# Kernel optimization log

Hardware: AMD Instinct MI355X
Metric: run time of the kernel (lower is better)

## Reference

```python
import jax, jax.numpy as jnp
import numpy as np

ROPE_THETA = 10000.0

def _rope(x, offset=0):
    # x: [B, H, T, d]; lucidrains rotary_embedding_torch interleaved-pair convention
    d = x.shape[-1]
    T = x.shape[-2]
    inv_freq = 1.0 / (ROPE_THETA ** (jnp.arange(0, d, 2, dtype=jnp.float32) / d))  # [d/2]
    t = jnp.arange(offset, offset + T, dtype=jnp.float32)
    freqs = t[:, None] * inv_freq[None, :]                 # [T, d/2]
    freqs = jnp.repeat(freqs, 2, axis=-1)                  # [T, d] (each freq duplicated for its pair)
    cos = jnp.cos(freqs).astype(x.dtype)
    sin = jnp.sin(freqs).astype(x.dtype)
    xr = x.reshape(*x.shape[:-1], d // 2, 2)
    x1, x2 = xr[..., 0], xr[..., 1]
    rot = jnp.stack([-x2, x1], axis=-1).reshape(x.shape)   # rotate_half, interleaved
    return x * cos + rot * sin


def setup_inputs() -> dict:
    key = jax.random.key(0)
    ks = jax.random.split(key, 5)
    B, T, C = 8, 1024, 1024
    s = 0.02
    x = jax.random.normal(ks[0], (B, T, C), dtype=jnp.float32)
    ipw = jax.random.normal(ks[1], (3 * C, C), dtype=jnp.float32) * s
    ipb = jax.random.normal(ks[2], (3 * C,), dtype=jnp.float32) * s
    opw = jax.random.normal(ks[3], (C, C), dtype=jnp.float32) * s
    opb = jax.random.normal(ks[4], (C,), dtype=jnp.float32) * s
    # bool mask, True = blocked (original code inverts before SDPA) -> causal
    causal_block = ~jnp.tril(jnp.ones((T, T), dtype=bool))
    attn_mask = causal_block[None, None, :, :]             # [1,1,T,T]
    return {"x": x, "ipw": ipw, "ipb": ipb, "opw": opw, "opb": opb,
            "attn_mask": attn_mask}


def reference(x, ipw, ipb, opw, opb, attn_mask):
    B, T, C = x.shape
    n_head = 16
    hd = C // n_head
    qkv = x @ ipw.T + ipb                                  # [B,T,3C]
    q, k, v = jnp.split(qkv, 3, axis=-1)
    def heads(z):
        return z.reshape(B, T, n_head, hd).transpose(0, 2, 1, 3)  # [B,H,T,hd]
    q, k, v = heads(q), heads(k), heads(v)
    q = _rope(q)
    k = _rope(k)
    scores = jnp.einsum('bhqd,bhkd->bhqk', q, k) / jnp.sqrt(jnp.asarray(hd, x.dtype))
    # attn_mask True = blocked; mask slice [FULL_T-T:FULL_T, :FULL_T] is the full mask here
    scores = jnp.where(attn_mask, jnp.asarray(-1e9, x.dtype), scores)
    attn = jax.nn.softmax(scores, axis=-1)
    y = jnp.einsum('bhqk,bhkd->bhqd', attn, v)             # [B,H,T,hd]
    y = y.transpose(0, 2, 1, 3).reshape(B, T, C)
    return y @ opw.T + opb
```

## Files before the change

kernel.cpp:

```cpp
#include <hip/hip_runtime.h>
#include <stdint.h>


typedef __bf16 bf16x8 __attribute__((ext_vector_type(8)));
typedef float f32x4 __attribute__((ext_vector_type(4)));
typedef __attribute__((address_space(1))) unsigned int as1_u32;
typedef __attribute__((address_space(3))) unsigned int as3_u32;

#define MFMA16(a, b, c) __builtin_amdgcn_mfma_f32_16x16x32_bf16((a), (b), (c), 0, 0, 0)

static __device__ __forceinline__ unsigned short f2bf(float f) {
    union { float f; unsigned u; } x; x.f = f;
    return (unsigned short)((x.u + 0x7fffu + ((x.u >> 16) & 1u)) >> 16);
}
static __device__ __forceinline__ float bf2f(unsigned short u) {
    union { unsigned u; float f; } x; x.u = ((unsigned)u) << 16;
    return x.f;
}
static __device__ __forceinline__ bf16x8 ld_bf16x8(const void* p) {
    return *(const bf16x8*)p;
}

__global__ void cast_f32_bf16(const float* __restrict__ in,
                              unsigned short* __restrict__ out, int n8) {
    int i = blockIdx.x * blockDim.x + threadIdx.x;
    if (i >= n8) return;
    float4 a = ((const float4*)in)[2 * i];
    float4 b = ((const float4*)in)[2 * i + 1];
    union { unsigned short us[8]; uint4 v; } o;
    o.us[0] = f2bf(a.x); o.us[1] = f2bf(a.y); o.us[2] = f2bf(a.z); o.us[3] = f2bf(a.w);
    o.us[4] = f2bf(b.x); o.us[5] = f2bf(b.y); o.us[6] = f2bf(b.z); o.us[7] = f2bf(b.w);
    ((uint4*)out)[i] = o.v;
}

__global__ void rope_table(float* __restrict__ ct, float* __restrict__ st) {
    int idx = blockIdx.x * blockDim.x + threadIdx.x;
    if (idx >= 1024 * 32) return;
    int t = idx >> 5, i = idx & 31;
    float inv = powf(10000.0f, -(float)(2 * i) * (1.0f / 64.0f));
    float f = (float)t * inv;
    ct[idx] = cosf(f);
    st[idx] = sinf(f);
}

template <int NC, bool OUT_BF16>
__global__ __launch_bounds__(256) void gemm_bt(const unsigned short* __restrict__ A,
                                               const unsigned short* __restrict__ W,
                                               const float* __restrict__ bias,
                                               void* __restrict__ Cout, int K) {
    __shared__ __attribute__((aligned(16))) unsigned short As[128 * 32];
    __shared__ __attribute__((aligned(16))) unsigned short Bs[128 * 32];

    constexpr int NT = NC / 128;
    int nwg = gridDim.x;
    int bid = blockIdx.x;
    int lg = (bid & 7) * (nwg >> 3) + (bid >> 3);
    int tm = lg / NT, tn = lg % NT;
    int m0 = tm * 128, n0 = tn * 128;

    int tid = threadIdx.x;
    int w = tid >> 6, l = tid & 63;
    int lr = l & 15, g = l >> 4;
    int ldsb = __builtin_amdgcn_readfirstlane(w * 512);

    int c0 = tid, c1 = tid + 256;
    const unsigned short* A0 = A + (size_t)(m0 + (c0 >> 2)) * K + (c0 & 3) * 8;
    const unsigned short* A1 = A + (size_t)(m0 + (c1 >> 2)) * K + (c1 & 3) * 8;
    const unsigned short* W0 = W + (size_t)(n0 + (c0 >> 2)) * K + (c0 & 3) * 8;
    const unsigned short* W1 = W + (size_t)(n0 + (c1 >> 2)) * K + (c1 & 3) * 8;

    f32x4 acc[4][4] = {};
    int wr = (w >> 1) * 64, wc = (w & 1) * 64;

    for (int k0 = 0; k0 < K; k0 += 32) {
        __syncthreads();
        __builtin_amdgcn_global_load_lds((const as1_u32*)(A0 + k0), (as3_u32*)(As + ldsb), 16, 0, 0);
        __builtin_amdgcn_global_load_lds((const as1_u32*)(A1 + k0), (as3_u32*)(As + 2048 + ldsb), 16, 0, 0);
        __builtin_amdgcn_global_load_lds((const as1_u32*)(W0 + k0), (as3_u32*)(Bs + ldsb), 16, 0, 0);
        __builtin_amdgcn_global_load_lds((const as1_u32*)(W1 + k0), (as3_u32*)(Bs + 2048 + ldsb), 16, 0, 0);
        __syncthreads();

        bf16x8 a[4], b[4];
#pragma unroll
        for (int i = 0; i < 4; ++i) a[i] = ld_bf16x8(As + (wr + i * 16 + lr) * 32 + g * 8);
#pragma unroll
        for (int j = 0; j < 4; ++j) b[j] = ld_bf16x8(Bs + (wc + j * 16 + lr) * 32 + g * 8);
#pragma unroll
        for (int i = 0; i < 4; ++i)
#pragma unroll
            for (int j = 0; j < 4; ++j) acc[i][j] = MFMA16(a[i], b[j], acc[i][j]);
    }

    int g4 = g * 4;
#pragma unroll
    for (int j = 0; j < 4; ++j) {
        int col = n0 + wc + j * 16 + lr;
        float bv = bias[col];
#pragma unroll
        for (int i = 0; i < 4; ++i) {
#pragma unroll
            for (int r = 0; r < 4; ++r) {
                int row = m0 + wr + i * 16 + g4 + r;
                float v = acc[i][j][r] + bv;
                if (OUT_BF16)
                    ((unsigned short*)Cout)[(size_t)row * NC + col] = f2bf(v);
                else
                    ((float*)Cout)[(size_t)row * NC + col] = v;
            }
        }
    }
}

__global__ void rope_reshape(const unsigned short* __restrict__ qkv,
                             const float* __restrict__ ct, const float* __restrict__ st,
                             unsigned short* __restrict__ Qh,
                             unsigned short* __restrict__ Kh,
                             unsigned short* __restrict__ Vh) {
    int idx = blockIdx.x * blockDim.x + threadIdx.x;
    if (idx >= 8192 * 384) return;
    int row = idx / 384;
    int c8 = idx - row * 384;
    int col = c8 * 8;
    int sec = col >> 10;
    int wi = col & 1023;
    int h = wi >> 6, d = wi & 63;
    int t = row & 1023;

    uint4 raw = *(const uint4*)(qkv + (size_t)row * 3072 + col);
    size_t obase = ((size_t)((row >> 10) * 16 + h) * 1024 + t) * 64 + d;

    if (sec == 2) {
        *(uint4*)(Vh + obase) = raw;
        return;
    }
    union { uint4 v; unsigned short us[8]; } u; u.v = raw;
    float x[8];
#pragma unroll
    for (int i = 0; i < 8; ++i) x[i] = bf2f(u.us[i]);
    float scale = (sec == 0) ? 0.125f : 1.0f;
    union { uint4 v; unsigned short us[8]; } o;
#pragma unroll
    for (int p = 0; p < 4; ++p) {
        int fi = t * 32 + (d >> 1) + p;
        float c = ct[fi], s = st[fi];
        float e0 = (x[2 * p] * c - x[2 * p + 1] * s) * scale;
        float e1 = (x[2 * p + 1] * c + x[2 * p] * s) * scale;
        o.us[2 * p] = f2bf(e0);
        o.us[2 * p + 1] = f2bf(e1);
    }
    unsigned short* dst = (sec == 0) ? Qh : Kh;
    *(uint4*)(dst + obase) = o.v;
}

__global__ __launch_bounds__(256) void attn_fwd(const unsigned short* __restrict__ Qh,
                                                const unsigned short* __restrict__ Kh,
                                                const unsigned short* __restrict__ Vh,
                                                unsigned short* __restrict__ Yb) {
    __shared__ __attribute__((aligned(16))) unsigned short Ks[64 * 64];
    __shared__ __attribute__((aligned(16))) unsigned short Vts[64 * 64];
    __shared__ __attribute__((aligned(16))) unsigned short Ps[4 * 16 * 64];

    int bid = blockIdx.x;
    int lg = (bid & 7) * 256 + (bid >> 3);
    int bh = lg >> 4;
    int qi = lg & 15;
    int q0 = qi * 64;

    int tid = threadIdx.x, w = tid >> 6, l = tid & 63;
    int lr = l & 15, g = l >> 4;
    int ldsb = __builtin_amdgcn_readfirstlane(w * 512);

    const unsigned short* Kbase = Kh + (size_t)bh * 65536;
    const unsigned short* Vbase = Vh + (size_t)bh * 65536;

    bf16x8 qf0, qf1;
    {
        const unsigned short* qp = Qh + (size_t)bh * 65536 + (size_t)(q0 + w * 16 + lr) * 64 + g * 8;
        qf0 = ld_bf16x8(qp);
        qf1 = ld_bf16x8(qp + 32);
    }

    f32x4 y[4] = {};
    float run_m[4], run_l[4];
#pragma unroll
    for (int r = 0; r < 4; ++r) { run_m[r] = -1e30f; run_l[r] = 0.0f; }

    int c0 = tid, c1 = tid + 256;
    const unsigned short* K0 = Kbase + (size_t)(c0 >> 3) * 64 + ((c0 ^ (c0 >> 3)) & 7) * 8;
    const unsigned short* K1 = Kbase + (size_t)(c1 >> 3) * 64 + ((c1 ^ (c1 >> 3)) & 7) * 8;
    int vr = tid >> 2, vd0 = (tid & 3) * 16;
    const unsigned short* V0 = Vbase + (size_t)vr * 64 + vd0;
    unsigned short* Pw = Ps + w * 1024;

    for (int j = 0; j <= qi; ++j) {
        int kvoff = j * 4096;
        __syncthreads();
        __builtin_amdgcn_global_load_lds((const as1_u32*)(K0 + kvoff), (as3_u32*)(Ks + ldsb), 16, 0, 0);
        __builtin_amdgcn_global_load_lds((const as1_u32*)(K1 + kvoff), (as3_u32*)(Ks + 2048 + ldsb), 16, 0, 0);
        uint4 v0 = *(const uint4*)(V0 + kvoff);
        uint4 v1 = *(const uint4*)(V0 + kvoff + 8);
        {
            union { uint4 v[2]; unsigned short us[16]; } u; u.v[0] = v0; u.v[1] = v1;
#pragma unroll
            for (int i = 0; i < 16; ++i) {
                int d = vd0 + i;
                int off = d * 128 + ((((vr >> 3) ^ d) & 7) << 4) + ((vr & 7) << 1);
                *(unsigned short*)((char*)Vts + off) = u.us[i];
            }
        }
        __syncthreads();

        f32x4 s[4];
#pragma unroll
        for (int nt = 0; nt < 4; ++nt) {
            int row = nt * 16 + lr;
            bf16x8 kf0 = ld_bf16x8((const char*)Ks + row * 128 + (((g + 0) ^ (row & 7)) << 4));
            bf16x8 kf1 = ld_bf16x8((const char*)Ks + row * 128 + (((g + 4) ^ (row & 7)) << 4));
            f32x4 z = {};
            z = MFMA16(qf0, kf0, z);
            z = MFMA16(qf1, kf1, z);
            s[nt] = z;
        }

        if (j == qi) {
#pragma unroll
            for (int nt = 0; nt < 4; ++nt) {
                int kv = nt * 16 + lr;
#pragma unroll
                for (int r = 0; r < 4; ++r) {
                    int qrow = w * 16 + g * 4 + r;
                    s[nt][r] = (kv > qrow) ? -1e30f : s[nt][r];
                }
            }
        }

#pragma unroll
        for (int r = 0; r < 4; ++r) {
            float tm_ = fmaxf(fmaxf(s[0][r], s[1][r]), fmaxf(s[2][r], s[3][r]));
            tm_ = fmaxf(tm_, __shfl_xor(tm_, 1));
            tm_ = fmaxf(tm_, __shfl_xor(tm_, 2));
            tm_ = fmaxf(tm_, __shfl_xor(tm_, 4));
            tm_ = fmaxf(tm_, __shfl_xor(tm_, 8));
            float nm = fmaxf(run_m[r], tm_);
            float alpha = __expf(run_m[r] - nm);
            run_m[r] = nm;
            float ts = 0.0f;
#pragma unroll
            for (int nt = 0; nt < 4; ++nt) {
                float pv = __expf(s[nt][r] - nm);
                s[nt][r] = pv;
                ts += pv;
            }
            ts += __shfl_xor(ts, 1);
            ts += __shfl_xor(ts, 2);
            ts += __shfl_xor(ts, 4);
            ts += __shfl_xor(ts, 8);
            run_l[r] = run_l[r] * alpha + ts;
#pragma unroll
            for (int nt = 0; nt < 4; ++nt) y[nt][r] *= alpha;
        }

#pragma unroll
        for (int nt = 0; nt < 4; ++nt)
#pragma unroll
            for (int r = 0; r < 4; ++r) {
                int m = g * 4 + r;
                int col = nt * 16 + lr;
                int off = m * 128 + ((((col >> 3) ^ m) & 7) << 4) + ((col & 7) << 1);
                *(unsigned short*)((char*)Pw + off) = f2bf(s[nt][r]);
            }

#pragma unroll
        for (int ks = 0; ks < 2; ++ks) {
            int slot = (g + ks * 4) ^ (lr & 7);
            bf16x8 pa = ld_bf16x8((const char*)Pw + lr * 128 + slot * 16);
#pragma unroll
            for (int nt = 0; nt < 4; ++nt) {
                int d = nt * 16 + lr;
                int vs = ((g + ks * 4) ^ d) & 7;
                bf16x8 vb = ld_bf16x8((const char*)Vts + d * 128 + (vs << 4));
                y[nt] = MFMA16(pa, vb, y[nt]);
            }
        }
    }

    int b = bh >> 4, h = bh & 15;
#pragma unroll
    for (int r = 0; r < 4; ++r) {
        float inv = 1.0f / run_l[r];
        int row = q0 + w * 16 + g * 4 + r;
        size_t obase = ((size_t)(b * 1024 + row)) * 1024 + h * 64;
#pragma unroll
        for (int nt = 0; nt < 4; ++nt) Yb[obase + nt * 16 + lr] = f2bf(y[nt][r] * inv);
    }
}

extern "C" void kernel_launch(void* const* d_in, const int* in_sizes, int n_in,
                              void* d_out, int out_size, void* d_ws, size_t ws_size,
                              hipStream_t stream) {
    const float* x = (const float*)d_in[0];
    const float* ipw = (const float*)d_in[1];
    const float* ipb = (const float*)d_in[2];
    const float* opw = (const float*)d_in[3];
    const float* opb = (const float*)d_in[4];

    char* ws = (char*)d_ws;
    unsigned short* xb   = (unsigned short*)(ws);
    unsigned short* wqkv = (unsigned short*)(ws + 16777216);
    unsigned short* wo   = (unsigned short*)(ws + 23068672);
    float* ct            = (float*)(ws + 25165824);
    float* st            = (float*)(ws + 25296896);
    unsigned short* qkvb = (unsigned short*)(ws + 25427968);
    unsigned short* Qh   = (unsigned short*)(ws + 75759616);
    unsigned short* Kh   = (unsigned short*)(ws + 92536832);
    unsigned short* Vh   = (unsigned short*)(ws + 109314048);
    unsigned short* yb   = (unsigned short*)(ws + 126091264);

    cast_f32_bf16<<<4096, 256, 0, stream>>>(x, xb, 1048576);
    cast_f32_bf16<<<1536, 256, 0, stream>>>(ipw, wqkv, 393216);
    cast_f32_bf16<<<512, 256, 0, stream>>>(opw, wo, 131072);
    rope_table<<<128, 256, 0, stream>>>(ct, st);

    gemm_bt<3072, true><<<1536, 256, 0, stream>>>(xb, wqkv, ipb, qkvb, 1024);
    rope_reshape<<<12288, 256, 0, stream>>>(qkvb, ct, st, Qh, Kh, Vh);
    attn_fwd<<<2048, 256, 0, stream>>>(Qh, Kh, Vh, yb);
    gemm_bt<1024, false><<<512, 256, 0, stream>>>(yb, wo, opb, d_out, 1024);
}
```

Before: 324.0 us.

## Pair causal query tiles per block, pre-transpose V, keep P in registers

The attention kernel now gives each block two query tiles (p and 15-p), so causal work is balanced across blocks and each loaded K/V tile is reused by both. V is transposed into a separate buffer by a new kernel, which lets it be loaded with direct global-to-LDS copies instead of scalar transposed LDS stores. Scores are computed as K·Q so the softmax probabilities stay in registers as the MFMA operand, removing the LDS round trip for P. Row reductions shrink to two shuffles, and the output is staged through LDS for coalesced stores. The cost is an extra transpose launch, more registers per thread and half as many blocks.

```diff
diff --git a/kernel.cpp b/kernel.cpp
--- a/kernel.cpp
+++ b/kernel.cpp
@@ -19,6 +19,11 @@
 }
 static __device__ __forceinline__ bf16x8 ld_bf16x8(const void* p) {
     return *(const bf16x8*)p;
+}
+static __device__ __forceinline__ unsigned cvtpk(float lo, float hi) {
+    unsigned r;
+    asm("v_cvt_pk_bf16_f32 %0, %1, %2" : "=v"(r) : "v"(lo), "v"(hi));
+    return r;
 }
 
 __global__ void cast_f32_bf16(const float* __restrict__ in,
@@ -114,13 +119,11 @@
 __global__ void rope_reshape(const unsigned short* __restrict__ qkv,
                              const float* __restrict__ ct, const float* __restrict__ st,
                              unsigned short* __restrict__ Qh,
-                             unsigned short* __restrict__ Kh,
-                             unsigned short* __restrict__ Vh) {
+                             unsigned short* __restrict__ Kh) {
     int idx = blockIdx.x * blockDim.x + threadIdx.x;
-    if (idx >= 8192 * 384) return;
-    int row = idx / 384;
-    int c8 = idx - row * 384;
-    int col = c8 * 8;
+    if (idx >= 8192 * 256) return;
+    int row = idx >> 8;
+    int col = (idx & 255) * 8;
     int sec = col >> 10;
     int wi = col & 1023;
     int h = wi >> 6, d = wi & 63;
@@ -129,10 +132,6 @@
     uint4 raw = *(const uint4*)(qkv + (size_t)row * 3072 + col);
     size_t obase = ((size_t)((row >> 10) * 16 + h) * 1024 + t) * 64 + d;
 
-    if (sec == 2) {
-        *(uint4*)(Vh + obase) = raw;
-        return;
-    }
     union { uint4 v; unsigned short us[8]; } u; u.v = raw;
     float x[8];
 #pragma unroll
@@ -152,147 +151,177 @@
     *(uint4*)(dst + obase) = o.v;
 }
 
+__global__ __launch_bounds__(256) void transpose_v(const unsigned short* __restrict__ qkv,
+                                                   unsigned short* __restrict__ Vt) {
+    __shared__ unsigned short Ts[64 * 67];
+    int bid = blockIdx.x;
+    int bh = bid >> 4, tt = bid & 15;
+    int b = bh >> 4, h = bh & 15;
+    int t0 = tt * 64;
+    int tid = threadIdx.x;
+#pragma unroll
+    for (int cc = 0; cc < 2; ++cc) {
+        int c = tid + cc * 256;
+        int trow = c >> 3, d8 = (c & 7) * 8;
+        uint4 v = *(const uint4*)(qkv + (size_t)(b * 1024 + t0 + trow) * 3072 + 2048 + h * 64 + d8);
+        union { uint4 v; unsigned short us[8]; } u; u.v = v;
+#pragma unroll
+        for (int i = 0; i < 8; ++i) Ts[trow * 67 + d8 + i] = u.us[i];
+    }
+    __syncthreads();
+#pragma unroll
+    for (int cc = 0; cc < 2; ++cc) {
+        int c = tid + cc * 256;
+        int drow = c >> 3, t8 = (c & 7) * 8;
+        union { uint4 v; unsigned short us[8]; } u;
+#pragma unroll
+        for (int i = 0; i < 8; ++i) u.us[i] = Ts[(t8 + i) * 67 + drow];
+        *(uint4*)(Vt + (size_t)bh * 65536 + (size_t)drow * 1024 + t0 + t8) = u.v;
+    }
+}
+
+__device__ __forceinline__ void attn_tile(const unsigned short* Ks, const unsigned short* Vs,
+                                          bf16x8 q0f, bf16x8 q1f, f32x4 (&y)[4],
+                                          float& rm, float& rl,
+                                          int lr, int g, bool diag, int wq) {
+    const char* kc = (const char*)Ks;
+    const char* vc = (const char*)Vs;
+    int l7 = lr & 7;
+    int kof0 = lr * 128 + ((g ^ l7) << 4);
+    int kof1 = lr * 128 + (((g + 4) ^ l7) << 4);
+    f32x4 s[4];
+#pragma unroll
+    for (int nt = 0; nt < 4; ++nt) {
+        bf16x8 kf0 = ld_bf16x8(kc + nt * 2048 + kof0);
+        bf16x8 kf1 = ld_bf16x8(kc + nt * 2048 + kof1);
+        f32x4 z = {};
+        z = MFMA16(kf0, q0f, z);
+        z = MFMA16(kf1, q1f, z);
+        s[nt] = z;
+    }
+    if (diag) {
+#pragma unroll
+        for (int nt = 0; nt < 4; ++nt)
+#pragma unroll
+            for (int r = 0; r < 4; ++r)
+                if (nt * 16 + g * 4 + r > wq + lr) s[nt][r] = -3e38f;
+    }
+    float tm;
+    {
+        f32x4 m4;
+#pragma unroll
+        for (int r = 0; r < 4; ++r) m4[r] = fmaxf(fmaxf(s[0][r], s[1][r]), fmaxf(s[2][r], s[3][r]));
+        tm = fmaxf(fmaxf(m4[0], m4[1]), fmaxf(m4[2], m4[3]));
+    }
+    tm = fmaxf(tm, __shfl_xor(tm, 16));
+    tm = fmaxf(tm, __shfl_xor(tm, 32));
+    float nm = fmaxf(rm, tm);
+    float alpha = __expf(rm - nm);
+    rm = nm;
+    float ts = 0.f;
+#pragma unroll
+    for (int nt = 0; nt < 4; ++nt)
+#pragma unroll
+        for (int r = 0; r < 4; ++r) { float pv = __expf(s[nt][r] - nm); s[nt][r] = pv; ts += pv; }
+    ts += __shfl_xor(ts, 16);
+    ts += __shfl_xor(ts, 32);
+    rl = rl * alpha + ts;
+#pragma unroll
+    for (int nt = 0; nt < 4; ++nt) y[nt] *= alpha;
+    union { unsigned u[4]; bf16x8 v; } pf0, pf1;
+    pf0.u[0] = cvtpk(s[0][0], s[0][1]); pf0.u[1] = cvtpk(s[0][2], s[0][3]);
+    pf0.u[2] = cvtpk(s[1][0], s[1][1]); pf0.u[3] = cvtpk(s[1][2], s[1][3]);
+    pf1.u[0] = cvtpk(s[2][0], s[2][1]); pf1.u[1] = cvtpk(s[2][2], s[2][3]);
+    pf1.u[2] = cvtpk(s[3][0], s[3][1]); pf1.u[3] = cvtpk(s[3][2], s[3][3]);
+    int s0 = g >> 1, h8 = (g & 1) * 8;
+    int vo0 = lr * 128 + h8 + (((s0 + 0) ^ l7) << 4);
+    int vo1 = lr * 128 + h8 + (((s0 + 2) ^ l7) << 4);
+    int vo2 = lr * 128 + h8 + (((s0 + 4) ^ l7) << 4);
+    int vo3 = lr * 128 + h8 + (((s0 + 6) ^ l7) << 4);
+#pragma unroll
+    for (int nt = 0; nt < 4; ++nt) {
+        union { uint2 u2[2]; bf16x8 v; } vf;
+        vf.u2[0] = *(const uint2*)(vc + nt * 2048 + vo0);
+        vf.u2[1] = *(const uint2*)(vc + nt * 2048 + vo1);
+        y[nt] = MFMA16(vf.v, pf0.v, y[nt]);
+        union { uint2 u2[2]; bf16x8 v; } vg;
+        vg.u2[0] = *(const uint2*)(vc + nt * 2048 + vo2);
+        vg.u2[1] = *(const uint2*)(vc + nt * 2048 + vo3);
+        y[nt] = MFMA16(vg.v, pf1.v, y[nt]);
+    }
+}
+
+__device__ __forceinline__ void attn_epilogue(unsigned short* smem, unsigned short* __restrict__ Yb,
+                                              f32x4 (&y)[4], float rl, int qtile,
+                                              int b, int hh, int w, int lr, int g, int tid) {
+    __syncthreads();
+    float inv = 1.0f / rl;
+    char* ep = (char*)smem;
+#pragma unroll
+    for (int nt = 0; nt < 4; ++nt) {
+        uint2 pr;
+        pr.x = cvtpk(y[nt][0] * inv, y[nt][1] * inv);
+        pr.y = cvtpk(y[nt][2] * inv, y[nt][3] * inv);
+        *(uint2*)(ep + (w * 16 + lr) * 144 + (nt * 16 + g * 4) * 2) = pr;
+    }
+    __syncthreads();
+    int q = tid >> 2, dc = (tid & 3) * 16;
+    uint4 u0 = *(const uint4*)(ep + q * 144 + dc * 2);
+    uint4 u1 = *(const uint4*)(ep + q * 144 + dc * 2 + 16);
+    size_t orow = ((size_t)(b * 1024 + qtile * 64 + q)) * 1024 + hh * 64 + dc;
+    *(uint4*)(Yb + orow) = u0;
+    *(uint4*)(Yb + orow + 8) = u1;
+}
+
 __global__ __launch_bounds__(256) void attn_fwd(const unsigned short* __restrict__ Qh,
                                                 const unsigned short* __restrict__ Kh,
-                                                const unsigned short* __restrict__ Vh,
+                                                const unsigned short* __restrict__ Vt,
                                                 unsigned short* __restrict__ Yb) {
-    __shared__ __attribute__((aligned(16))) unsigned short Ks[64 * 64];
-    __shared__ __attribute__((aligned(16))) unsigned short Vts[64 * 64];
-    __shared__ __attribute__((aligned(16))) unsigned short Ps[4 * 16 * 64];
+    __shared__ __attribute__((aligned(16))) unsigned short smem[8192];
+    unsigned short* Ks = smem;
+    unsigned short* Vs = smem + 4096;
 
     int bid = blockIdx.x;
-    int lg = (bid & 7) * 256 + (bid >> 3);
-    int bh = lg >> 4;
-    int qi = lg & 15;
-    int q0 = qi * 64;
+    int lg = (bid & 7) * 128 + (bid >> 3);
+    int bh = lg >> 3, p = lg & 7;
+    int qa = p, qb = 15 - p;
 
     int tid = threadIdx.x, w = tid >> 6, l = tid & 63;
     int lr = l & 15, g = l >> 4;
     int ldsb = __builtin_amdgcn_readfirstlane(w * 512);
 
-    const unsigned short* Kbase = Kh + (size_t)bh * 65536;
-    const unsigned short* Vbase = Vh + (size_t)bh * 65536;
-
-    bf16x8 qf0, qf1;
-    {
-        const unsigned short* qp = Qh + (size_t)bh * 65536 + (size_t)(q0 + w * 16 + lr) * 64 + g * 8;
-        qf0 = ld_bf16x8(qp);
-        qf1 = ld_bf16x8(qp + 32);
-    }
-
-    f32x4 y[4] = {};
-    float run_m[4], run_l[4];
-#pragma unroll
-    for (int r = 0; r < 4; ++r) { run_m[r] = -1e30f; run_l[r] = 0.0f; }
+    size_t bh64 = (size_t)bh * 65536;
+    const unsigned short* qbase = Qh + bh64 + (size_t)(w * 16 + lr) * 64 + g * 8;
+    bf16x8 qA0 = ld_bf16x8(qbase + qa * 4096);
+    bf16x8 qA1 = ld_bf16x8(qbase + qa * 4096 + 32);
+    bf16x8 qB0 = ld_bf16x8(qbase + qb * 4096);
+    bf16x8 qB1 = ld_bf16x8(qbase + qb * 4096 + 32);
+
+    f32x4 yA[4] = {}, yB[4] = {};
+    float mA = -3e38f, lA = 0.f, mB = -3e38f, lB = 0.f;
 
     int c0 = tid, c1 = tid + 256;
-    const unsigned short* K0 = Kbase + (size_t)(c0 >> 3) * 64 + ((c0 ^ (c0 >> 3)) & 7) * 8;
-    const unsigned short* K1 = Kbase + (size_t)(c1 >> 3) * 64 + ((c1 ^ (c1 >> 3)) & 7) * 8;
-    int vr = tid >> 2, vd0 = (tid & 3) * 16;
-    const unsigned short* V0 = Vbase + (size_t)vr * 64 + vd0;
-    unsigned short* Pw = Ps + w * 1024;
-
-    for (int j = 0; j <= qi; ++j) {
-        int kvoff = j * 4096;
+    const unsigned short* K0 = Kh + bh64 + (c0 >> 3) * 64 + ((c0 ^ (c0 >> 3)) & 7) * 8;
+    const unsigned short* K1 = Kh + bh64 + (c1 >> 3) * 64 + ((c1 ^ (c1 >> 3)) & 7) * 8;
+    const unsigned short* V0 = Vt + bh64 + (c0 >> 3) * 1024 + ((c0 ^ (c0 >> 3)) & 7) * 8;
+    const unsigned short* V1 = Vt + bh64 + (c1 >> 3) * 1024 + ((c1 ^ (c1 >> 3)) & 7) * 8;
+
+    for (int t = 0; t <= qb; ++t) {
         __syncthreads();
-        __builtin_amdgcn_global_load_lds((const as1_u32*)(K0 + kvoff), (as3_u32*)(Ks + ldsb), 16, 0, 0);
-        __builtin_amdgcn_global_load_lds((const as1_u32*)(K1 + kvoff), (as3_u32*)(Ks + 2048 + ldsb), 16, 0, 0);
-        uint4 v0 = *(const uint4*)(V0 + kvoff);
-        uint4 v1 = *(const uint4*)(V0 + kvoff + 8);
-        {
-            union { uint4 v[2]; unsigned short us[16]; } u; u.v[0] = v0; u.v[1] = v1;
-#pragma unroll
-            for (int i = 0; i < 16; ++i) {
-                int d = vd0 + i;
-                int off = d * 128 + ((((vr >> 3) ^ d) & 7) << 4) + ((vr & 7) << 1);
-                *(unsigned short*)((char*)Vts + off) = u.us[i];
-            }
-        }
+        __builtin_amdgcn_global_load_lds((const as1_u32*)(K0 + t * 4096), (as3_u32*)(Ks + ldsb), 16, 0, 0);
+        __builtin_amdgcn_global_load_lds((const as1_u32*)(K1 + t * 4096), (as3_u32*)(Ks + 2048 + ldsb), 16, 0, 0);
+        __builtin_amdgcn_global_load_lds((const as1_u32*)(V0 + t * 64), (as3_u32*)(Vs + ldsb), 16, 0, 0);
+        __builtin_amdgcn_global_load_lds((const as1_u32*)(V1 + t * 64), (as3_u32*)(Vs + 2048 + ldsb), 16, 0, 0);
         __syncthreads();
 
-        f32x4 s[4];
-#pragma unroll
-        for (int nt = 0; nt < 4; ++nt) {
-            int row = nt * 16 + lr;
-            bf16x8 kf0 = ld_bf16x8((const char*)Ks + row * 128 + (((g + 0) ^ (row & 7)) << 4));
-            bf16x8 kf1 = ld_bf16x8((const char*)Ks + row * 128 + (((g + 4) ^ (row & 7)) << 4));
-            f32x4 z = {};
-            z = MFMA16(qf0, kf0, z);
-            z = MFMA16(qf1, kf1, z);
-            s[nt] = z;
-        }
-
-        if (j == qi) {
-#pragma unroll
-            for (int nt = 0; nt < 4; ++nt) {
-                int kv = nt * 16 + lr;
-#pragma unroll
-                for (int r = 0; r < 4; ++r) {
-                    int qrow = w * 16 + g * 4 + r;
-                    s[nt][r] = (kv > qrow) ? -1e30f : s[nt][r];
-                }
-            }
-        }
-
-#pragma unroll
-        for (int r = 0; r < 4; ++r) {
-            float tm_ = fmaxf(fmaxf(s[0][r], s[1][r]), fmaxf(s[2][r], s[3][r]));
-            tm_ = fmaxf(tm_, __shfl_xor(tm_, 1));
-            tm_ = fmaxf(tm_, __shfl_xor(tm_, 2));
-            tm_ = fmaxf(tm_, __shfl_xor(tm_, 4));
-            tm_ = fmaxf(tm_, __shfl_xor(tm_, 8));
-            float nm = fmaxf(run_m[r], tm_);
-            float alpha = __expf(run_m[r] - nm);
-            run_m[r] = nm;
-            float ts = 0.0f;
-#pragma unroll
-            for (int nt = 0; nt < 4; ++nt) {
-                float pv = __expf(s[nt][r] - nm);
-                s[nt][r] = pv;
-                ts += pv;
-            }
-            ts += __shfl_xor(ts, 1);
-            ts += __shfl_xor(ts, 2);
-            ts += __shfl_xor(ts, 4);
-            ts += __shfl_xor(ts, 8);
-            run_l[r] = run_l[r] * alpha + ts;
-#pragma unroll
-            for (int nt = 0; nt < 4; ++nt) y[nt][r] *= alpha;
-        }
-
-#pragma unroll
-        for (int nt = 0; nt < 4; ++nt)
-#pragma unroll
-            for (int r = 0; r < 4; ++r) {
-                int m = g * 4 + r;
-                int col = nt * 16 + lr;
-                int off = m * 128 + ((((col >> 3) ^ m) & 7) << 4) + ((col & 7) << 1);
-                *(unsigned short*)((char*)Pw + off) = f2bf(s[nt][r]);
-            }
-
-#pragma unroll
-        for (int ks = 0; ks < 2; ++ks) {
-            int slot = (g + ks * 4) ^ (lr & 7);
-            bf16x8 pa = ld_bf16x8((const char*)Pw + lr * 128 + slot * 16);
-#pragma unroll
-            for (int nt = 0; nt < 4; ++nt) {
-                int d = nt * 16 + lr;
-                int vs = ((g + ks * 4) ^ d) & 7;
-                bf16x8 vb = ld_bf16x8((const char*)Vts + d * 128 + (vs << 4));
-                y[nt] = MFMA16(pa, vb, y[nt]);
-            }
-        }
-    }
-
-    int b = bh >> 4, h = bh & 15;
-#pragma unroll
-    for (int r = 0; r < 4; ++r) {
-        float inv = 1.0f / run_l[r];
-        int row = q0 + w * 16 + g * 4 + r;
-        size_t obase = ((size_t)(b * 1024 + row)) * 1024 + h * 64;
-#pragma unroll
-        for (int nt = 0; nt < 4; ++nt) Yb[obase + nt * 16 + lr] = f2bf(y[nt][r] * inv);
-    }
+        if (t <= qa)
+            attn_tile(Ks, Vs, qA0, qA1, yA, mA, lA, lr, g, t == qa, w * 16);
+        attn_tile(Ks, Vs, qB0, qB1, yB, mB, lB, lr, g, t == qb, w * 16);
+    }
+
+    int b = bh >> 4, hh = bh & 15;
+    attn_epilogue(smem, Yb, yA, lA, qa, b, hh, w, lr, g, tid);
+    attn_epilogue(smem, Yb, yB, lB, qb, b, hh, w, lr, g, tid);
 }
 
 extern "C" void kernel_launch(void* const* d_in, const int* in_sizes, int n_in,
@@ -313,7 +342,7 @@
     unsigned short* qkvb = (unsigned short*)(ws + 25427968);
     unsigned short* Qh   = (unsigned short*)(ws + 75759616);
     unsigned short* Kh   = (unsigned short*)(ws + 92536832);
-    unsigned short* Vh   = (unsigned short*)(ws + 109314048);
+    unsigned short* Vt   = (unsigned short*)(ws + 109314048);
     unsigned short* yb   = (unsigned short*)(ws + 126091264);
 
     cast_f32_bf16<<<4096, 256, 0, stream>>>(x, xb, 1048576);
@@ -322,7 +351,8 @@
     rope_table<<<128, 256, 0, stream>>>(ct, st);
 
     gemm_bt<3072, true><<<1536, 256, 0, stream>>>(xb, wqkv, ipb, qkvb, 1024);
-    rope_reshape<<<12288, 256, 0, stream>>>(qkvb, ct, st, Qh, Kh, Vh);
-    attn_fwd<<<2048, 256, 0, stream>>>(Qh, Kh, Vh, yb);
+    rope_reshape<<<8192, 256, 0, stream>>>(qkvb, ct, st, Qh, Kh);
+    transpose_v<<<2048, 256, 0, stream>>>(qkvb, Vt);
+    attn_fwd<<<1024, 256, 0, stream>>>(Qh, Kh, Vt, yb);
     gemm_bt<1024, false><<<512, 256, 0, stream>>>(yb, wo, opb, d_out, 1024);
 }
```

New measurement: 285.8 us. 1.13x faster.
